# Performance work log

Measured on AMD Instinct MI355X. Metric: run time of the kernel, lower is better.

Reference implementation:

```python
import jax, jax.numpy as jnp
import numpy as np

DIM = 1024
HEADS = 16
HEAD_DIM = DIM // HEADS


def setup_inputs() -> dict:
    key = jax.random.key(0)
    ks = jax.random.split(key, 5)
    B, N = 4, 2048
    x = jax.random.normal(ks[0], (B, N, DIM), dtype=jnp.float32)
    # nn.Linear default init scale ~ 1/sqrt(fan_in)
    s = 1.0 / np.sqrt(DIM)
    W_qkv = jax.random.uniform(ks[1], (DIM, 3 * DIM), minval=-s, maxval=s, dtype=jnp.float32)
    b_qkv = jax.random.uniform(ks[2], (3 * DIM,), minval=-s, maxval=s, dtype=jnp.float32)
    W_proj = jax.random.uniform(ks[3], (DIM, DIM), minval=-s, maxval=s, dtype=jnp.float32)
    b_proj = jax.random.uniform(ks[4], (DIM,), minval=-s, maxval=s, dtype=jnp.float32)
    return {"x": x, "W_qkv": W_qkv, "b_qkv": b_qkv, "W_proj": W_proj, "b_proj": b_proj}


def reference(x, W_qkv, b_qkv, W_proj, b_proj):
    B, N, C = x.shape
    qkv = x @ W_qkv + b_qkv                      # [B, N, 3C]
    qkv = qkv.reshape(B, N, 3, HEADS, HEAD_DIM)
    q = jnp.transpose(qkv[:, :, 0], (0, 2, 1, 3))  # [B, H, N, D]
    k = jnp.transpose(qkv[:, :, 1], (0, 2, 1, 3))
    v = jnp.transpose(qkv[:, :, 2], (0, 2, 1, 3))
    scale = 1.0 / np.sqrt(HEAD_DIM)
    scores = jnp.einsum('bhqd,bhkd->bhqk', q, k) * scale  # [B, H, N, N]
    attn = jax.nn.softmax(scores, axis=-1)
    out = jnp.einsum('bhqk,bhkd->bhqd', attn, v)           # [B, H, N, D]
    out = jnp.transpose(out, (0, 2, 1, 3)).reshape(B, N, C)
    return out @ W_proj + b_proj
```

## Files before the change

### kernel.cpp

```cpp
#include <hip/hip_runtime.h>

typedef __attribute__((ext_vector_type(2)))  float  f32x2;
typedef __attribute__((ext_vector_type(4)))  float  f32x4;
typedef __attribute__((ext_vector_type(16))) float  f32x16;
typedef __attribute__((ext_vector_type(8)))  short  short8;
typedef __attribute__((ext_vector_type(4)))  unsigned int u32x4;
typedef __attribute__((ext_vector_type(2)))  unsigned int uint2v;

#define MFMA16 __builtin_amdgcn_mfma_f32_16x16x32_bf16
#define MFMA32 __builtin_amdgcn_mfma_f32_32x32x16_bf16

static __device__ __forceinline__ unsigned short f2bf(float f){
  union { float f; unsigned u; } v; v.f = f;
  unsigned r = v.u + 0x7fffu + ((v.u >> 16) & 1u);
  return (unsigned short)(r >> 16);
}

static __device__ __forceinline__ unsigned cvtpk(float a, float b){
  unsigned r;
  asm("v_cvt_pk_bf16_f32 %0, %1, %2" : "=v"(r) : "v"(a), "v"(b));
  return r;
}

static __device__ __forceinline__ void plswap(unsigned &a, unsigned &b){
  asm("v_permlane32_swap_b32 %0, %1" : "+v"(a), "+v"(b));
}

typedef __attribute__((address_space(1))) void gvoid_t;
typedef __attribute__((address_space(3))) void lvoid_t;

static __device__ __forceinline__ void gll16(const unsigned short* g, unsigned short* l){
  __builtin_amdgcn_global_load_lds((gvoid_t*)g, (lvoid_t*)l, 16, 0, 0);
}


__global__ __launch_bounds__(256) void k_convert(const float* __restrict__ x,
                                                 unsigned short* __restrict__ xb){
  __shared__ __align__(16) unsigned short sm[16384];
  const int mblk = blockIdx.x >> 4, kt = blockIdx.x & 15;
  const int t = threadIdx.x;
  const int l16 = t & 15, rg = t >> 4;
  #pragma unroll
  for (int p = 0; p < 16; p++){
    int row = p * 16 + rg;
    f32x4 v = *(const f32x4*)&x[(size_t)(mblk*256 + row) * 1024 + kt*64 + l16*4];
    uint2v u; u[0] = cvtpk(v[0], v[1]); u[1] = cvtpk(v[2], v[3]);
    int g = l16 >> 1;
    *(uint2v*)&sm[row*64 + ((g ^ (row & 7)) << 3) + (l16 & 1)*4] = u;
  }
  __syncthreads();
  size_t obase = (size_t)((mblk*16 + kt)*2) * 8192;
  #pragma unroll
  for (int i = 0; i < 8; i++){
    int o = i * 256 + t;
    int kh = o >> 10, rem = o & 1023;
    int band = rem >> 6, cc = (rem >> 4) & 3, ri = rem & 15;
    int r = band*16 + ri, g = kh*4 + cc;
    short8 vv = *(const short8*)&sm[r*64 + ((g ^ (r & 7)) << 3)];
    *(short8*)&xb[obase + (size_t)kh*8192 + rem*8] = vv;
  }
}

__global__ __launch_bounds__(256) void k_transpose(const float* __restrict__ W,
                                                   unsigned short* __restrict__ Wt,
                                                   int K, int N){
  __shared__ float tile[32][33];
  int n0 = blockIdx.x * 32, k0 = blockIdx.y * 32;
  int tx = threadIdx.x, ty = threadIdx.y;
  #pragma unroll
  for (int r = 0; r < 4; r++)
    tile[ty + 8*r][tx] = W[(size_t)(k0 + ty + 8*r) * N + n0 + tx];
  __syncthreads();
  #pragma unroll
  for (int r = 0; r < 4; r++){
    int nn = ty + 8*r;
    int n = n0 + nn, k = k0 + tx;
    int kt = k >> 6, kh = (k >> 5) & 1, cc = (k >> 3) & 3, ke = k & 7;
    int nblk = n >> 8, band = (n & 255) >> 4, ri = n & 15;
    Wt[(size_t)(((nblk*16 + kt)*2 + kh)) * 8192 + band*512 + cc*128 + ri*8 + ke] =
        f2bf(tile[tx][nn]);
  }
}

#define VMW(N) { __builtin_amdgcn_sched_barrier(0);                        \
                 asm volatile("s_waitcnt vmcnt(" #N ")" ::: "memory");     \
                 __builtin_amdgcn_s_barrier();                             \
                 __builtin_amdgcn_sched_barrier(0); }

template<int MODE>
__global__ __launch_bounds__(512, 2) void k_gemm(const unsigned short* __restrict__ A,
                                                 const unsigned short* __restrict__ Bt,
                                                 const float* __restrict__ bias,
                                                 void* __restrict__ outp,
                                                 int NT){
  __shared__ __align__(16) unsigned short lds[49152];
  const int t = threadIdx.x, w = t >> 6, l = t & 63;
  const int wr = w >> 2, wc = w & 3;
  const int bx = blockIdx.x, by = blockIdx.y;
  const int mblk = bx >> 1, mhalf = bx & 1;

  const unsigned short* Ab = A + (size_t)mblk*262144 + mhalf*4096 + t*8;
  const unsigned short* Bb = Bt + (size_t)by*262144 + t*8;

  f32x4 acc[4][4];
  #pragma unroll
  for (int i = 0; i < 4; i++)
    #pragma unroll
    for (int j = 0; j < 4; j++)
      acc[i][j] = (f32x4){0.f, 0.f, 0.f, 0.f};

  auto stage = [&](int sl){
    const int b = sl & 3;
    const size_t off = (size_t)sl * 8192;
    gll16(Ab + off,        &lds[b*12288 + t*8]);
    gll16(Bb + off,        &lds[b*12288 + 4096 + t*8]);
    gll16(Bb + off + 4096, &lds[b*12288 + 8192 + t*8]);
  };

  auto phase = [&](int b, bool do_stage, int sl){
    short8 af[4], bfr[4];
    const int aoff = b*12288 + wr*2048 + l*8;
    const int boff = b*12288 + 4096 + wc*2048 + l*8;
    #pragma unroll
    for (int i = 0; i < 4; i++) af[i]  = *(const short8*)&lds[aoff + i*512];
    #pragma unroll
    for (int j = 0; j < 4; j++) bfr[j] = *(const short8*)&lds[boff + j*512];
    if (do_stage) stage(sl);
    __builtin_amdgcn_sched_barrier(0);
    __builtin_amdgcn_s_barrier();
    __builtin_amdgcn_s_setprio(1);
    #pragma unroll
    for (int i = 0; i < 4; i++)
      #pragma unroll
      for (int j = 0; j < 4; j++)
        acc[i][j] = MFMA16(af[i], bfr[j], acc[i][j], 0, 0, 0);
    __builtin_amdgcn_s_setprio(0);
  };

  stage(0); stage(1); stage(2);
  VMW(6);

  const int NP = 2 * NT;
  int p = 0;
  for (; p <= NP - 4; ++p){
    phase(p & 3, true, p + 3);
    VMW(6);
  }
  phase(p & 3, false, 0); VMW(3); ++p;
  phase(p & 3, false, 0); VMW(0); ++p;
  phase(p & 3, false, 0);

  if (MODE == 0){
    unsigned short* qg = (unsigned short*)outp;
    unsigned short* kg = qg + (size_t)8388608;
    unsigned short* vg = kg + (size_t)8388608;
    const int which = by >> 2;
    const int lrow = l & 15;
    #pragma unroll
    for (int j = 0; j < 4; j++){
      int col = by*256 + wc*64 + j*16 + lrow;
      float bi = bias[col];
      int cc = col & 1023;
      int h = cc >> 6;
      int d = j*16 + lrow;
      if (which == 2){
        int db = d >> 5, dd = d & 31;
        #pragma unroll
        for (int i = 0; i < 4; i++){
          int nn = bx*128 + wr*64 + i*16 + (l >> 4)*4;
          int b = nn >> 11, key = nn & 2047;
          size_t idx = (size_t)(key >> 6)*4096 + (size_t)(((key >> 4) & 3)*2 + db)*512
                     + (((key >> 3) & 1)*32 + dd)*8 + (key & 7);
          uint2v u;
          u[0] = cvtpk(acc[i][j][0] + bi, acc[i][j][1] + bi);
          u[1] = cvtpk(acc[i][j][2] + bi, acc[i][j][3] + bi);
          *(uint2v*)&vg[(size_t)(b*16 + h)*131072 + idx] = u;
        }
      } else {
        unsigned short* dst = which ? kg : qg;
        float scale = which ? 1.0f : 0.18033688011f;
        int dsub = (d >> 4)*512 + ((d >> 3) & 1)*256 + (d & 7);
        #pragma unroll
        for (int i = 0; i < 4; i++)
          #pragma unroll
          for (int reg = 0; reg < 4; reg++){
            int nn = bx*128 + wr*64 + i*16 + (l >> 4)*4 + reg;
            int b = nn >> 11, row = nn & 2047;
            dst[(size_t)(b*16 + h)*131072 + (size_t)(row >> 5)*2048 + dsub + (row & 31)*8] =
                f2bf((acc[i][j][reg] + bi) * scale);
          }
      }
    }
  } else {
    float* out = (float*)outp;
    #pragma unroll
    for (int i = 0; i < 4; i++)
      #pragma unroll
      for (int reg = 0; reg < 4; reg++){
        int row = bx*128 + wr*64 + i*16 + (l >> 4)*4 + reg;
        #pragma unroll
        for (int j = 0; j < 4; j++){
          int col = by*256 + wc*64 + j*16 + (l & 15);
          out[(size_t)row * 1024 + col] = acc[i][j][reg] + bias[col];
        }
      }
  }
}

__global__ __launch_bounds__(256, 4) void k_attn(const unsigned short* __restrict__ Qg,
                                                 const unsigned short* __restrict__ Kg,
                                                 const unsigned short* __restrict__ Vg,
                                                 unsigned short* __restrict__ aout){
  __shared__ __align__(16) unsigned short lds[16384];

  const int t = threadIdx.x, w = t >> 6, l = t & 63;
  const int hi = l >> 5, q31 = l & 31;
  const int d0 = blockIdx.x;
  const int xcd = d0 & 7, jj = d0 >> 3;
  const int bh = xcd + 8*(jj >> 4);
  const int bx = jj & 15;

  const unsigned short* Qp = Qg + (size_t)bh*131072 + (size_t)bx*8192;
  const unsigned short* Kp = Kg + (size_t)bh*131072;
  const unsigned short* Vp = Vg + (size_t)bh*131072;

  #pragma unroll
  for (int i = 0; i < 4; i++){ int c = i*256 + t; gll16(Qp + c*8, &lds[c*8]); }
  __syncthreads();
  short8 qf[4];
  #pragma unroll
  for (int ds = 0; ds < 4; ds++)
    qf[ds] = *(const short8*)&lds[(w*4 + ds)*512 + l*8];
  __syncthreads();

  #pragma unroll
  for (int i = 0; i < 2; i++){
    int c = i*256 + t;
    gll16(Kp + c*8, &lds[c*8]);
    gll16(Vp + c*8, &lds[4096 + c*8]);
  }
  __syncthreads();

  f32x16 oacc0, oacc1;
  #pragma unroll
  for (int i = 0; i < 16; i++){ oacc0[i] = 0.f; oacc1[i] = 0.f; }
  float lsum = 0.f;

  for (int kt = 0; kt < 32; kt++){
    const int cb = (kt & 1) * 8192;
    if (kt < 31){
      const int nb = cb ^ 8192;
      #pragma unroll
      for (int i = 0; i < 2; i++){
        int c = i*256 + t;
        gll16(Kp + (size_t)(kt + 1)*4096 + c*8, &lds[nb + c*8]);
        gll16(Vp + (size_t)(kt + 1)*4096 + c*8, &lds[nb + 4096 + c*8]);
      }
    }

    f32x16 sA, sB;
    #pragma unroll
    for (int i = 0; i < 16; i++){ sA[i] = 0.f; sB[i] = 0.f; }
    __builtin_amdgcn_s_setprio(1);
    #pragma unroll
    for (int ds = 0; ds < 4; ds++){
      short8 kfA = *(const short8*)&lds[cb + ds*512 + l*8];
      short8 kfB = *(const short8*)&lds[cb + 2048 + ds*512 + l*8];
      sA = MFMA32(kfA, qf[ds], sA, 0, 0, 0);
      sB = MFMA32(kfB, qf[ds], sB, 0, 0, 0);
    }
    __builtin_amdgcn_s_setprio(0);

    #pragma unroll
    for (int i = 0; i < 16; i++){
      sA[i] = __builtin_amdgcn_exp2f(sA[i]);
      sB[i] = __builtin_amdgcn_exp2f(sB[i]);
    }
    f32x2 a2[8], b2[8];
    #pragma unroll
    for (int j = 0; j < 8; j++){
      a2[j][0] = sA[2*j]; a2[j][1] = sA[2*j+1];
      b2[j][0] = sB[2*j]; b2[j][1] = sB[2*j+1];
    }
    f32x2 s2v = ((a2[0] + a2[1]) + (a2[2] + a2[3])) + ((a2[4] + a2[5]) + (a2[6] + a2[7]))
              + ((b2[0] + b2[1]) + (b2[2] + b2[3])) + ((b2[4] + b2[5]) + (b2[6] + b2[7]));
    float rs = s2v[0] + s2v[1];
    rs += __shfl_xor(rs, 32);
    lsum += rs;

    unsigned wA[8], wB[8];
    #pragma unroll
    for (int j = 0; j < 8; j++){
      wA[j] = cvtpk(a2[j][0], a2[j][1]);
      wB[j] = cvtpk(b2[j][0], b2[j][1]);
    }
    u32x4 pf[4];
    { unsigned a = wA[0], b = wA[2]; plswap(a, b); pf[0][0] = a; pf[0][2] = b; }
    { unsigned a = wA[1], b = wA[3]; plswap(a, b); pf[0][1] = a; pf[0][3] = b; }
    { unsigned a = wA[4], b = wA[6]; plswap(a, b); pf[1][0] = a; pf[1][2] = b; }
    { unsigned a = wA[5], b = wA[7]; plswap(a, b); pf[1][1] = a; pf[1][3] = b; }
    { unsigned a = wB[0], b = wB[2]; plswap(a, b); pf[2][0] = a; pf[2][2] = b; }
    { unsigned a = wB[1], b = wB[3]; plswap(a, b); pf[2][1] = a; pf[2][3] = b; }
    { unsigned a = wB[4], b = wB[6]; plswap(a, b); pf[3][0] = a; pf[3][2] = b; }
    { unsigned a = wB[5], b = wB[7]; plswap(a, b); pf[3][1] = a; pf[3][3] = b; }

    __builtin_amdgcn_s_setprio(1);
    #pragma unroll
    for (int ks = 0; ks < 4; ks++){
      short8 pfr;
      *(u32x4*)&pfr = pf[ks];
      short8 vf0 = *(const short8*)&lds[cb + 4096 + (ks*2 + 0)*512 + l*8];
      short8 vf1 = *(const short8*)&lds[cb + 4096 + (ks*2 + 1)*512 + l*8];
      oacc0 = MFMA32(vf0, pfr, oacc0, 0, 0, 0);
      oacc1 = MFMA32(vf1, pfr, oacc1, 0, 0, 0);
    }
    __builtin_amdgcn_s_setprio(0);

    __syncthreads();
  }

  {
    float inv = 1.0f / lsum;
    int qrow = w*32 + q31;
    #pragma unroll
    for (int j = 0; j < 8; j++){
      int dd0 = 8*(j >> 1) + 2*(j & 1) + 4*hi;
      unsigned u0 = cvtpk(oacc0[2*j] * inv, oacc0[2*j+1] * inv);
      *(unsigned*)&lds[qrow*64 + (((dd0 >> 3) ^ (qrow & 7)) << 3) + (dd0 & 7)] = u0;
      int dd1 = dd0 + 32;
      unsigned u1 = cvtpk(oacc1[2*j] * inv, oacc1[2*j+1] * inv);
      *(unsigned*)&lds[qrow*64 + (((dd1 >> 3) ^ (qrow & 7)) << 3) + (dd1 & 7)] = u1;
    }
  }
  __syncthreads();
  {
    int mblk16 = (bh >> 4)*8 + (bx >> 1);
    int h = bh & 15;
    int bandbase = 8*(bx & 1);
    #pragma unroll
    for (int i = 0; i < 4; i++){
      int idx = i*256 + t;
      int kh = idx >> 9, band_l = (idx >> 6) & 7, cc = (idx >> 4) & 3, ri = idx & 15;
      int r = band_l*16 + ri, g = kh*4 + cc;
      short8 vv = *(const short8*)&lds[r*64 + ((g ^ (r & 7)) << 3)];
      size_t chunk = (size_t)((mblk16*16 + h)*2 + kh);
      *(short8*)&aout[chunk*8192 + (size_t)(bandbase + band_l)*512 + cc*128 + ri*8] = vv;
    }
  }
}

extern "C" void kernel_launch(void* const* d_in, const int* in_sizes, int n_in,
                              void* d_out, int out_size, void* d_ws, size_t ws_size,
                              hipStream_t stream){
  const float* x     = (const float*)d_in[0];
  const float* Wqkv  = (const float*)d_in[1];
  const float* bqkv  = (const float*)d_in[2];
  const float* Wproj = (const float*)d_in[3];
  const float* bproj = (const float*)d_in[4];

  unsigned short* ws   = (unsigned short*)d_ws;
  unsigned short* xb   = ws;
  unsigned short* Wqt  = ws + (size_t)8192 * 1024;
  unsigned short* Wpt  = Wqt + (size_t)3072 * 1024;
  unsigned short* qkvb = Wpt + (size_t)1024 * 1024;

  k_convert<<<512, 256, 0, stream>>>(x, xb);
  k_transpose<<<dim3(96, 32), dim3(32, 8), 0, stream>>>(Wqkv, Wqt, 1024, 3072);
  k_transpose<<<dim3(32, 32), dim3(32, 8), 0, stream>>>(Wproj, Wpt, 1024, 1024);
  k_gemm<0><<<dim3(64, 12), 512, 0, stream>>>(xb, Wqt, bqkv, qkvb, 16);
  k_attn<<<1024, 256, 0, stream>>>(qkvb, qkvb + (size_t)8388608,
                                   qkvb + (size_t)16777216, xb);
  k_gemm<1><<<dim3(64, 4), 512, 0, stream>>>(xb, Wpt, bproj, (void*)d_out, 16);
}
```

Before: 174.0 us.

## Process two Q tiles per wave in attention to reuse K/V fragments

```diff
diff --git a/kernel.cpp b/kernel.cpp
--- a/kernel.cpp
+++ b/kernel.cpp
@@ -207,7 +207,7 @@
   }
 }
 
-__global__ __launch_bounds__(256, 4) void k_attn(const unsigned short* __restrict__ Qg,
+__global__ __launch_bounds__(256, 2) void k_attn(const unsigned short* __restrict__ Qg,
                                                  const unsigned short* __restrict__ Kg,
                                                  const unsigned short* __restrict__ Vg,
                                                  unsigned short* __restrict__ aout){
@@ -217,20 +217,22 @@
   const int hi = l >> 5, q31 = l & 31;
   const int d0 = blockIdx.x;
   const int xcd = d0 & 7, jj = d0 >> 3;
-  const int bh = xcd + 8*(jj >> 4);
-  const int bx = jj & 15;
-
-  const unsigned short* Qp = Qg + (size_t)bh*131072 + (size_t)bx*8192;
+  const int bh = xcd + 8*(jj >> 3);
+  const int bx = jj & 7;
+
+  const unsigned short* Qp = Qg + (size_t)bh*131072 + (size_t)bx*16384;
   const unsigned short* Kp = Kg + (size_t)bh*131072;
   const unsigned short* Vp = Vg + (size_t)bh*131072;
 
   #pragma unroll
-  for (int i = 0; i < 4; i++){ int c = i*256 + t; gll16(Qp + c*8, &lds[c*8]); }
-  __syncthreads();
-  short8 qf[4];
-  #pragma unroll
-  for (int ds = 0; ds < 4; ds++)
-    qf[ds] = *(const short8*)&lds[(w*4 + ds)*512 + l*8];
+  for (int i = 0; i < 8; i++){ int c = i*256 + t; gll16(Qp + c*8, &lds[c*8]); }
+  __syncthreads();
+  short8 qf0[4], qf1[4];
+  #pragma unroll
+  for (int ds = 0; ds < 4; ds++){
+    qf0[ds] = *(const short8*)&lds[(2*w + 0)*2048 + ds*512 + l*8];
+    qf1[ds] = *(const short8*)&lds[(2*w + 1)*2048 + ds*512 + l*8];
+  }
   __syncthreads();
 
   #pragma unroll
@@ -241,10 +243,10 @@
   }
   __syncthreads();
 
-  f32x16 oacc0, oacc1;
-  #pragma unroll
-  for (int i = 0; i < 16; i++){ oacc0[i] = 0.f; oacc1[i] = 0.f; }
-  float lsum = 0.f;
+  f32x16 o0lo, o0hi, o1lo, o1hi;
+  #pragma unroll
+  for (int i = 0; i < 16; i++){ o0lo[i]=0.f; o0hi[i]=0.f; o1lo[i]=0.f; o1hi[i]=0.f; }
+  float lsum0 = 0.f, lsum1 = 0.f;
 
   for (int kt = 0; kt < 32; kt++){
     const int cb = (kt & 1) * 8192;
@@ -258,61 +260,83 @@
       }
     }
 
-    f32x16 sA, sB;
-    #pragma unroll
-    for (int i = 0; i < 16; i++){ sA[i] = 0.f; sB[i] = 0.f; }
+    f32x16 sA0, sB0, sA1, sB1;
+    #pragma unroll
+    for (int i = 0; i < 16; i++){ sA0[i]=0.f; sB0[i]=0.f; sA1[i]=0.f; sB1[i]=0.f; }
     __builtin_amdgcn_s_setprio(1);
     #pragma unroll
     for (int ds = 0; ds < 4; ds++){
       short8 kfA = *(const short8*)&lds[cb + ds*512 + l*8];
       short8 kfB = *(const short8*)&lds[cb + 2048 + ds*512 + l*8];
-      sA = MFMA32(kfA, qf[ds], sA, 0, 0, 0);
-      sB = MFMA32(kfB, qf[ds], sB, 0, 0, 0);
+      sA0 = MFMA32(kfA, qf0[ds], sA0, 0, 0, 0);
+      sB0 = MFMA32(kfB, qf0[ds], sB0, 0, 0, 0);
+      sA1 = MFMA32(kfA, qf1[ds], sA1, 0, 0, 0);
+      sB1 = MFMA32(kfB, qf1[ds], sB1, 0, 0, 0);
     }
     __builtin_amdgcn_s_setprio(0);
 
     #pragma unroll
     for (int i = 0; i < 16; i++){
-      sA[i] = __builtin_amdgcn_exp2f(sA[i]);
-      sB[i] = __builtin_amdgcn_exp2f(sB[i]);
-    }
-    f32x2 a2[8], b2[8];
-    #pragma unroll
-    for (int j = 0; j < 8; j++){
-      a2[j][0] = sA[2*j]; a2[j][1] = sA[2*j+1];
-      b2[j][0] = sB[2*j]; b2[j][1] = sB[2*j+1];
-    }
-    f32x2 s2v = ((a2[0] + a2[1]) + (a2[2] + a2[3])) + ((a2[4] + a2[5]) + (a2[6] + a2[7]))
-              + ((b2[0] + b2[1]) + (b2[2] + b2[3])) + ((b2[4] + b2[5]) + (b2[6] + b2[7]));
-    float rs = s2v[0] + s2v[1];
-    rs += __shfl_xor(rs, 32);
-    lsum += rs;
-
-    unsigned wA[8], wB[8];
-    #pragma unroll
-    for (int j = 0; j < 8; j++){
-      wA[j] = cvtpk(a2[j][0], a2[j][1]);
-      wB[j] = cvtpk(b2[j][0], b2[j][1]);
-    }
-    u32x4 pf[4];
-    { unsigned a = wA[0], b = wA[2]; plswap(a, b); pf[0][0] = a; pf[0][2] = b; }
-    { unsigned a = wA[1], b = wA[3]; plswap(a, b); pf[0][1] = a; pf[0][3] = b; }
-    { unsigned a = wA[4], b = wA[6]; plswap(a, b); pf[1][0] = a; pf[1][2] = b; }
-    { unsigned a = wA[5], b = wA[7]; plswap(a, b); pf[1][1] = a; pf[1][3] = b; }
-    { unsigned a = wB[0], b = wB[2]; plswap(a, b); pf[2][0] = a; pf[2][2] = b; }
-    { unsigned a = wB[1], b = wB[3]; plswap(a, b); pf[2][1] = a; pf[2][3] = b; }
-    { unsigned a = wB[4], b = wB[6]; plswap(a, b); pf[3][0] = a; pf[3][2] = b; }
-    { unsigned a = wB[5], b = wB[7]; plswap(a, b); pf[3][1] = a; pf[3][3] = b; }
+      sA0[i] = __builtin_amdgcn_exp2f(sA0[i]);
+      sB0[i] = __builtin_amdgcn_exp2f(sB0[i]);
+      sA1[i] = __builtin_amdgcn_exp2f(sA1[i]);
+      sB1[i] = __builtin_amdgcn_exp2f(sB1[i]);
+    }
+    {
+      float r0 = (((sA0[0]+sA0[1])+(sA0[2]+sA0[3])) + ((sA0[4]+sA0[5])+(sA0[6]+sA0[7])))
+               + (((sA0[8]+sA0[9])+(sA0[10]+sA0[11])) + ((sA0[12]+sA0[13])+(sA0[14]+sA0[15])))
+               + (((sB0[0]+sB0[1])+(sB0[2]+sB0[3])) + ((sB0[4]+sB0[5])+(sB0[6]+sB0[7])))
+               + (((sB0[8]+sB0[9])+(sB0[10]+sB0[11])) + ((sB0[12]+sB0[13])+(sB0[14]+sB0[15])));
+      r0 += __shfl_xor(r0, 32);
+      lsum0 += r0;
+      float r1 = (((sA1[0]+sA1[1])+(sA1[2]+sA1[3])) + ((sA1[4]+sA1[5])+(sA1[6]+sA1[7])))
+               + (((sA1[8]+sA1[9])+(sA1[10]+sA1[11])) + ((sA1[12]+sA1[13])+(sA1[14]+sA1[15])))
+               + (((sB1[0]+sB1[1])+(sB1[2]+sB1[3])) + ((sB1[4]+sB1[5])+(sB1[6]+sB1[7])))
+               + (((sB1[8]+sB1[9])+(sB1[10]+sB1[11])) + ((sB1[12]+sB1[13])+(sB1[14]+sB1[15])));
+      r1 += __shfl_xor(r1, 32);
+      lsum1 += r1;
+    }
+
+    u32x4 pf0[4], pf1[4];
+    {
+      unsigned wA[8], wB[8];
+      #pragma unroll
+      for (int j = 0; j < 8; j++){ wA[j] = cvtpk(sA0[2*j], sA0[2*j+1]); wB[j] = cvtpk(sB0[2*j], sB0[2*j+1]); }
+      { unsigned a=wA[0],b=wA[2]; plswap(a,b); pf0[0][0]=a; pf0[0][2]=b; }
+      { unsigned a=wA[1],b=wA[3]; plswap(a,b); pf0[0][1]=a; pf0[0][3]=b; }
+      { unsigned a=wA[4],b=wA[6]; plswap(a,b); pf0[1][0]=a; pf0[1][2]=b; }
+      { unsigned a=wA[5],b=wA[7]; plswap(a,b); pf0[1][1]=a; pf0[1][3]=b; }
+      { unsigned a=wB[0],b=wB[2]; plswap(a,b); pf0[2][0]=a; pf0[2][2]=b; }
+      { unsigned a=wB[1],b=wB[3]; plswap(a,b); pf0[2][1]=a; pf0[2][3]=b; }
+      { unsigned a=wB[4],b=wB[6]; plswap(a,b); pf0[3][0]=a; pf0[3][2]=b; }
+      { unsigned a=wB[5],b=wB[7]; plswap(a,b); pf0[3][1]=a; pf0[3][3]=b; }
+    }
+    {
+      unsigned wA[8], wB[8];
+      #pragma unroll
+      for (int j = 0; j < 8; j++){ wA[j] = cvtpk(sA1[2*j], sA1[2*j+1]); wB[j] = cvtpk(sB1[2*j], sB1[2*j+1]); }
+      { unsigned a=wA[0],b=wA[2]; plswap(a,b); pf1[0][0]=a; pf1[0][2]=b; }
+      { unsigned a=wA[1],b=wA[3]; plswap(a,b); pf1[0][1]=a; pf1[0][3]=b; }
+      { unsigned a=wA[4],b=wA[6]; plswap(a,b); pf1[1][0]=a; pf1[1][2]=b; }
+      { unsigned a=wA[5],b=wA[7]; plswap(a,b); pf1[1][1]=a; pf1[1][3]=b; }
+      { unsigned a=wB[0],b=wB[2]; plswap(a,b); pf1[2][0]=a; pf1[2][2]=b; }
+      { unsigned a=wB[1],b=wB[3]; plswap(a,b); pf1[2][1]=a; pf1[2][3]=b; }
+      { unsigned a=wB[4],b=wB[6]; plswap(a,b); pf1[3][0]=a; pf1[3][2]=b; }
+      { unsigned a=wB[5],b=wB[7]; plswap(a,b); pf1[3][1]=a; pf1[3][3]=b; }
+    }
 
     __builtin_amdgcn_s_setprio(1);
     #pragma unroll
     for (int ks = 0; ks < 4; ks++){
-      short8 pfr;
-      *(u32x4*)&pfr = pf[ks];
+      short8 p0r, p1r;
+      *(u32x4*)&p0r = pf0[ks];
+      *(u32x4*)&p1r = pf1[ks];
       short8 vf0 = *(const short8*)&lds[cb + 4096 + (ks*2 + 0)*512 + l*8];
       short8 vf1 = *(const short8*)&lds[cb + 4096 + (ks*2 + 1)*512 + l*8];
-      oacc0 = MFMA32(vf0, pfr, oacc0, 0, 0, 0);
-      oacc1 = MFMA32(vf1, pfr, oacc1, 0, 0, 0);
+      o0lo = MFMA32(vf0, p0r, o0lo, 0, 0, 0);
+      o0hi = MFMA32(vf1, p0r, o0hi, 0, 0, 0);
+      o1lo = MFMA32(vf0, p1r, o1lo, 0, 0, 0);
+      o1hi = MFMA32(vf1, p1r, o1hi, 0, 0, 0);
     }
     __builtin_amdgcn_s_setprio(0);
 
@@ -320,31 +344,35 @@
   }
 
   {
-    float inv = 1.0f / lsum;
-    int qrow = w*32 + q31;
+    float inv0 = 1.0f / lsum0, inv1 = 1.0f / lsum1;
+    int qr0 = w*64 + q31, qr1 = w*64 + 32 + q31;
     #pragma unroll
     for (int j = 0; j < 8; j++){
       int dd0 = 8*(j >> 1) + 2*(j & 1) + 4*hi;
-      unsigned u0 = cvtpk(oacc0[2*j] * inv, oacc0[2*j+1] * inv);
-      *(unsigned*)&lds[qrow*64 + (((dd0 >> 3) ^ (qrow & 7)) << 3) + (dd0 & 7)] = u0;
       int dd1 = dd0 + 32;
-      unsigned u1 = cvtpk(oacc1[2*j] * inv, oacc1[2*j+1] * inv);
-      *(unsigned*)&lds[qrow*64 + (((dd1 >> 3) ^ (qrow & 7)) << 3) + (dd1 & 7)] = u1;
+      *(unsigned*)&lds[qr0*64 + (((dd0 >> 3) ^ (qr0 & 7)) << 3) + (dd0 & 7)] =
+          cvtpk(o0lo[2*j] * inv0, o0lo[2*j+1] * inv0);
+      *(unsigned*)&lds[qr0*64 + (((dd1 >> 3) ^ (qr0 & 7)) << 3) + (dd1 & 7)] =
+          cvtpk(o0hi[2*j] * inv0, o0hi[2*j+1] * inv0);
+      *(unsigned*)&lds[qr1*64 + (((dd0 >> 3) ^ (qr1 & 7)) << 3) + (dd0 & 7)] =
+          cvtpk(o1lo[2*j] * inv1, o1lo[2*j+1] * inv1);
+      *(unsigned*)&lds[qr1*64 + (((dd1 >> 3) ^ (qr1 & 7)) << 3) + (dd1 & 7)] =
+          cvtpk(o1hi[2*j] * inv1, o1hi[2*j+1] * inv1);
     }
   }
   __syncthreads();
   {
-    int mblk16 = (bh >> 4)*8 + (bx >> 1);
+    int mblk = (bh >> 4)*8 + bx;
     int h = bh & 15;
-    int bandbase = 8*(bx & 1);
-    #pragma unroll
-    for (int i = 0; i < 4; i++){
+    #pragma unroll
+    for (int i = 0; i < 8; i++){
       int idx = i*256 + t;
-      int kh = idx >> 9, band_l = (idx >> 6) & 7, cc = (idx >> 4) & 3, ri = idx & 15;
-      int r = band_l*16 + ri, g = kh*4 + cc;
+      int kh = idx >> 10, rem = idx & 1023;
+      int band = rem >> 6, cc = (rem >> 4) & 3, ri = rem & 15;
+      int r = band*16 + ri, g = kh*4 + cc;
       short8 vv = *(const short8*)&lds[r*64 + ((g ^ (r & 7)) << 3)];
-      size_t chunk = (size_t)((mblk16*16 + h)*2 + kh);
-      *(short8*)&aout[chunk*8192 + (size_t)(bandbase + band_l)*512 + cc*128 + ri*8] = vv;
+      size_t chunk = (size_t)((mblk*16 + h)*2 + kh);
+      *(short8*)&aout[chunk*8192 + (size_t)band*512 + cc*128 + ri*8] = vv;
     }
   }
 }
@@ -368,7 +396,7 @@
   k_transpose<<<dim3(96, 32), dim3(32, 8), 0, stream>>>(Wqkv, Wqt, 1024, 3072);
   k_transpose<<<dim3(32, 32), dim3(32, 8), 0, stream>>>(Wproj, Wpt, 1024, 1024);
   k_gemm<0><<<dim3(64, 12), 512, 0, stream>>>(xb, Wqt, bqkv, qkvb, 16);
-  k_attn<<<1024, 256, 0, stream>>>(qkvb, qkvb + (size_t)8388608,
-                                   qkvb + (size_t)16777216, xb);
+  k_attn<<<512, 256, 0, stream>>>(qkvb, qkvb + (size_t)8388608,
+                                  qkvb + (size_t)16777216, xb);
   k_gemm<1><<<dim3(64, 4), 512, 0, stream>>>(xb, Wpt, bproj, (void*)d_out, 16);
 }
```

New measurement: 168.3 us. 3.3% less time.
